# Performance work log

Measured on AMD Instinct MI355X. Metric: run time of the kernel, lower is better.

The kernel has to match this reference:

```python
import jax, jax.numpy as jnp
import numpy as np

GRID = 32
GBOUND = 0.5
GRID_MIN = -GBOUND + GBOUND / GRID  # as in point2voxel


def _voxel_index(points):
    # points: [B,N,3] -> linear voxel indices [B,N]
    vx = (points - GRID_MIN) * GRID / (2.0 * GBOUND)
    vx = jnp.round(jnp.clip(vx, 0.0, GRID - 1))
    lin = vx @ jnp.array([GRID * GRID, GRID, 1], dtype=vx.dtype)
    return lin.astype(jnp.int32)


def _distance_loss(points, cps, v):
    # points [B,N,3], cps [B,G^3,3], v [B,G^3]
    lin = _voxel_index(points)                               # [B,N]
    mask = 1.0 - jnp.take_along_axis(v, lin, axis=1)         # [B,N]
    idx3 = jnp.broadcast_to(lin[:, :, None], lin.shape + (3,))
    gathered = jnp.take_along_axis(cps, idx3, axis=1)        # [B,N,3]
    d = (points - gathered) * mask[:, :, None]
    n2 = jnp.sum(d * d, axis=2)
    norm = jnp.sqrt(jnp.maximum(n2, 1e-30))                  # safe L2 norm
    return jnp.mean(jnp.sum(norm, axis=1))


def _plane_point(p, plane):
    # p [B,N,3], plane [B,1,4] -> reflected points [B,N,3]
    length = 2.0 * (jnp.sum(p * plane[..., :3], axis=2, keepdims=True) + plane[..., 3:4])
    norm2 = jnp.sum(plane[..., :3] ** 2, axis=2, keepdims=True)
    return p - length * plane[..., :3] / (norm2 + 1e-8)


def _quat_mul(q1, q2):
    w1, x1, y1, z1 = q1[..., 0], q1[..., 1], q1[..., 2], q1[..., 3]
    w2, x2, y2, z2 = q2[..., 0], q2[..., 1], q2[..., 2], q2[..., 3]
    w = w1 * w2 - x1 * x2 - y1 * y2 - z1 * z2
    x = w1 * x2 + x1 * w2 + y1 * z2 - z1 * y2
    y = w1 * y2 - x1 * z2 + y1 * w2 + z1 * x2
    z = w1 * z2 + x1 * y2 - y1 * x2 + z1 * w2
    return jnp.stack([w, x, y, z], axis=-1)


def _rotate_point(p, q):
    # p [B,N,3], q [B,1,4]
    B, N, _ = p.shape
    pq = jnp.concatenate([jnp.zeros((B, N, 1), p.dtype), p], axis=-1)
    qc = q * jnp.array([1.0, -1.0, -1.0, -1.0], q.dtype)
    return _quat_mul(_quat_mul(q, pq), qc)[..., 1:]


def setup_inputs() -> dict:
    key = jax.random.key(0)
    k = jax.random.split(key, 5)
    S, B, N, G = 3, 512, 1000, 32
    return {
        "planes": jax.random.normal(k[0], (S, B, 4), dtype=jnp.float32),
        "quats": jax.random.normal(k[1], (S, B, 4), dtype=jnp.float32),
        "closestPoints": jax.random.normal(k[2], (B, G ** 3 * 3), dtype=jnp.float32),
        "surfaceSamples": jax.random.normal(k[3], (B, N, 3), dtype=jnp.float32),
        "volume": jax.random.uniform(k[4], (B, 1, G, G, G), dtype=jnp.float32),
    }


def reference(planes, quats, closestPoints, surfaceSamples, volume):
    B = volume.shape[0]
    v = volume.reshape(B, GRID ** 3)
    cps = closestPoints.reshape(B, -1, 3)

    def per_sym(plane, quat):
        pl = plane[:, None, :]  # [B,1,4]
        lp = _distance_loss(_plane_point(surfaceSamples, pl), cps, v)
        qt = quat[:, None, :]
        lq = _distance_loss(_rotate_point(surfaceSamples, qt), cps, v)
        return lp, lq

    lps, lqs = jax.vmap(per_sym)(planes, quats)  # vectorized over S symmetry elems
    # sum over S then / S == mean, matching the torch loop
    return jnp.mean(lps), jnp.mean(lqs)
```

## Files before the change

### kernel.cpp

```cpp
#include <hip/hip_runtime.h>
#include <math.h>


#define NGRID3     32768
#define GRID_MIN_F (-0.484375f)
#define NTHREADS   256

__device__ __forceinline__ float point_loss(float x, float y, float z,
                                            const float* __restrict__ vol,
                                            const float* __restrict__ cp)
{
    float fx = fminf(fmaxf((x - GRID_MIN_F) * 32.0f, 0.0f), 31.0f);
    float fy = fminf(fmaxf((y - GRID_MIN_F) * 32.0f, 0.0f), 31.0f);
    float fz = fminf(fmaxf((z - GRID_MIN_F) * 32.0f, 0.0f), 31.0f);
    int lin = ((int)rintf(fx)) * 1024 + ((int)rintf(fy)) * 32 + (int)rintf(fz);

    float m  = 1.0f - vol[lin];
    float dx = (x - cp[lin * 3 + 0]) * m;
    float dy = (y - cp[lin * 3 + 1]) * m;
    float dz = (z - cp[lin * 3 + 2]) * m;
    return sqrtf(fmaxf(dx * dx + dy * dy + dz * dz, 1e-30f));
}

template <int S>
__global__ __launch_bounds__(NTHREADS) void symloss_fused(
    const float* __restrict__ planes,
    const float* __restrict__ quats,
    const float* __restrict__ cps,
    const float* __restrict__ samples,
    const float* __restrict__ volume,
    float* __restrict__ out,
    int B, int N, float scale)
{
    const int b = blockIdx.x;
    const float* __restrict__ vol = volume + (size_t)b * NGRID3;
    const float* __restrict__ cp  = cps    + (size_t)b * NGRID3 * 3;

    extern __shared__ float spts[];
    {
        const float* sp = samples + (size_t)b * N * 3;
        const int n4 = (N * 3) / 4;
        const float4* src = (const float4*)sp;
        float4* dst = (float4*)spts;
        for (int i = threadIdx.x; i < n4; i += NTHREADS) dst[i] = src[i];
        for (int i = n4 * 4 + threadIdx.x; i < N * 3; i += NTHREADS) spts[i] = sp[i];
    }

    float plx[S], ply[S], plz[S], plw[S], inv_n2[S];
    float qw[S], qx[S], qy[S], qz[S], w2mu[S];
#pragma unroll
    for (int s = 0; s < S; ++s) {
        float4 pl = ((const float4*)planes)[(size_t)s * B + b];
        float4 q  = ((const float4*)quats )[(size_t)s * B + b];
        plx[s] = pl.x; ply[s] = pl.y; plz[s] = pl.z; plw[s] = pl.w;
        inv_n2[s] = 1.0f / (pl.x * pl.x + pl.y * pl.y + pl.z * pl.z + 1e-8f);
        qw[s] = q.x; qx[s] = q.y; qy[s] = q.z; qz[s] = q.w;
        w2mu[s] = q.x * q.x - (q.y * q.y + q.z * q.z + q.w * q.w);
    }

    __syncthreads();

    float sum_p = 0.0f, sum_q = 0.0f;
    for (int n = threadIdx.x; n < N; n += NTHREADS) {
        const float px = spts[n * 3 + 0];
        const float py = spts[n * 3 + 1];
        const float pz = spts[n * 3 + 2];
#pragma unroll
        for (int s = 0; s < S; ++s) {
            float f = 2.0f * (px * plx[s] + py * ply[s] + pz * plz[s] + plw[s]) * inv_n2[s];
            sum_p += point_loss(px - f * plx[s], py - f * ply[s], pz - f * plz[s], vol, cp);

            float udp = qx[s] * px + qy[s] * py + qz[s] * pz;
            float cx  = qy[s] * pz - qz[s] * py;
            float cy  = qz[s] * px - qx[s] * pz;
            float cz  = qx[s] * py - qy[s] * px;
            sum_q += point_loss(w2mu[s] * px + 2.0f * (udp * qx[s] + qw[s] * cx),
                                w2mu[s] * py + 2.0f * (udp * qy[s] + qw[s] * cy),
                                w2mu[s] * pz + 2.0f * (udp * qz[s] + qw[s] * cz),
                                vol, cp);
        }
    }

    for (int off = 32; off > 0; off >>= 1) {
        sum_p += __shfl_down(sum_p, off);
        sum_q += __shfl_down(sum_q, off);
    }
    __shared__ float red[NTHREADS / 64][2];
    const int lane = threadIdx.x & 63;
    const int wid  = threadIdx.x >> 6;
    if (lane == 0) { red[wid][0] = sum_p; red[wid][1] = sum_q; }
    __syncthreads();

    if (threadIdx.x == 0) {
        float tp = 0.0f, tq = 0.0f;
        for (int w = 0; w < NTHREADS / 64; ++w) { tp += red[w][0]; tq += red[w][1]; }
        atomicAdd(&out[0], tp * scale);
        atomicAdd(&out[1], tq * scale);
    }
}

extern "C" void kernel_launch(void* const* d_in, const int* in_sizes, int n_in,
                              void* d_out, int out_size, void* d_ws, size_t ws_size,
                              hipStream_t stream)
{
    const float* planes  = (const float*)d_in[0];
    const float* quats   = (const float*)d_in[1];
    const float* cps     = (const float*)d_in[2];
    const float* samples = (const float*)d_in[3];
    const float* volume  = (const float*)d_in[4];
    float* out = (float*)d_out;

    const int B = in_sizes[4] / NGRID3;
    const int S = in_sizes[0] / (B * 4);
    const int N = in_sizes[3] / (B * 3);
    const float scale = 1.0f / (float)(S * B);
    const size_t lds = (size_t)N * 3 * sizeof(float);

    hipMemsetAsync(d_out, 0, 2 * sizeof(float), stream);

    switch (S) {
    case 1: symloss_fused<1><<<B, NTHREADS, lds, stream>>>(planes, quats, cps, samples, volume, out, B, N, scale); break;
    case 2: symloss_fused<2><<<B, NTHREADS, lds, stream>>>(planes, quats, cps, samples, volume, out, B, N, scale); break;
    case 3: symloss_fused<3><<<B, NTHREADS, lds, stream>>>(planes, quats, cps, samples, volume, out, B, N, scale); break;
    case 4: symloss_fused<4><<<B, NTHREADS, lds, stream>>>(planes, quats, cps, samples, volume, out, B, N, scale); break;
    default:
        for (int s = 0; s < S; ++s)
            symloss_fused<1><<<B, NTHREADS, lds, stream>>>(planes + (size_t)s * B * 4,
                                                           quats  + (size_t)s * B * 4,
                                                           cps, samples, volume, out, B, N, scale);
        break;
    }
}
```

Baseline: 303.1 us.

## Split each batch over point chunks and reduce partials in a second kernel

Launches C*B blocks, each handling one 256-point chunk of one batch element, instead of one block per batch element. Points are read straight from global memory, so the LDS staging and the barrier go away. Per-block partials go to the workspace and a single-block double-precision reduction kernel replaces the atomics and the memset. The aim is more parallelism to hide the latency of the scattered gathers into the volume and closest-point arrays. The cost is a second launch and less reuse, since blocks working on the same batch element now sit on different CUs.

Measured after the change: 302.0 us. No clear change (-0.3%).

```diff
diff --git a/kernel.cpp b/kernel.cpp
--- a/kernel.cpp
+++ b/kernel.cpp
@@ -16,35 +16,29 @@
     int lin = ((int)rintf(fx)) * 1024 + ((int)rintf(fy)) * 32 + (int)rintf(fz);
 
     float m  = 1.0f - vol[lin];
-    float dx = (x - cp[lin * 3 + 0]) * m;
-    float dy = (y - cp[lin * 3 + 1]) * m;
-    float dz = (z - cp[lin * 3 + 2]) * m;
+    int  c3  = lin * 3;
+    float dx = (x - cp[c3 + 0]) * m;
+    float dy = (y - cp[c3 + 1]) * m;
+    float dz = (z - cp[c3 + 2]) * m;
     return sqrtf(fmaxf(dx * dx + dy * dy + dz * dz, 1e-30f));
 }
 
 template <int S>
-__global__ __launch_bounds__(NTHREADS) void symloss_fused(
+__global__ __launch_bounds__(NTHREADS, 4) void symloss_stage1(
     const float* __restrict__ planes,
     const float* __restrict__ quats,
     const float* __restrict__ cps,
     const float* __restrict__ samples,
     const float* __restrict__ volume,
-    float* __restrict__ out,
-    int B, int N, float scale)
+    float* __restrict__ partials,
+    int B, int N)
 {
-    const int b = blockIdx.x;
+    const int bid = blockIdx.x;
+    const int b   = bid % B;
+    const int c   = bid / B;
+
     const float* __restrict__ vol = volume + (size_t)b * NGRID3;
     const float* __restrict__ cp  = cps    + (size_t)b * NGRID3 * 3;
-
-    extern __shared__ float spts[];
-    {
-        const float* sp = samples + (size_t)b * N * 3;
-        const int n4 = (N * 3) / 4;
-        const float4* src = (const float4*)sp;
-        float4* dst = (float4*)spts;
-        for (int i = threadIdx.x; i < n4; i += NTHREADS) dst[i] = src[i];
-        for (int i = n4 * 4 + threadIdx.x; i < N * 3; i += NTHREADS) spts[i] = sp[i];
-    }
 
     float plx[S], ply[S], plz[S], plw[S], inv_n2[S];
     float qw[S], qx[S], qy[S], qz[S], w2mu[S];
@@ -58,13 +52,13 @@
         w2mu[s] = q.x * q.x - (q.y * q.y + q.z * q.z + q.w * q.w);
     }
 
-    __syncthreads();
-
     float sum_p = 0.0f, sum_q = 0.0f;
-    for (int n = threadIdx.x; n < N; n += NTHREADS) {
-        const float px = spts[n * 3 + 0];
-        const float py = spts[n * 3 + 1];
-        const float pz = spts[n * 3 + 2];
+    const int n = c * NTHREADS + (int)threadIdx.x;
+    if (n < N) {
+        const float* sp = samples + ((size_t)b * N + n) * 3;
+        const float px = sp[0];
+        const float py = sp[1];
+        const float pz = sp[2];
 #pragma unroll
         for (int s = 0; s < S; ++s) {
             float f = 2.0f * (px * plx[s] + py * ply[s] + pz * plz[s] + plw[s]) * inv_n2[s];
@@ -94,8 +88,34 @@
     if (threadIdx.x == 0) {
         float tp = 0.0f, tq = 0.0f;
         for (int w = 0; w < NTHREADS / 64; ++w) { tp += red[w][0]; tq += red[w][1]; }
-        atomicAdd(&out[0], tp * scale);
-        atomicAdd(&out[1], tq * scale);
+        partials[2 * bid + 0] = tp;
+        partials[2 * bid + 1] = tq;
+    }
+}
+
+__global__ __launch_bounds__(NTHREADS) void symloss_reduce(
+    const float* __restrict__ partials, int M, float scale,
+    float* __restrict__ out)
+{
+    double sp = 0.0, sq = 0.0;
+    for (int i = threadIdx.x; i < M; i += NTHREADS) {
+        sp += (double)partials[2 * i + 0];
+        sq += (double)partials[2 * i + 1];
+    }
+    for (int off = 32; off > 0; off >>= 1) {
+        sp += __shfl_down(sp, off);
+        sq += __shfl_down(sq, off);
+    }
+    __shared__ double red[NTHREADS / 64][2];
+    const int lane = threadIdx.x & 63;
+    const int wid  = threadIdx.x >> 6;
+    if (lane == 0) { red[wid][0] = sp; red[wid][1] = sq; }
+    __syncthreads();
+    if (threadIdx.x == 0) {
+        double tp = 0.0, tq = 0.0;
+        for (int w = 0; w < NTHREADS / 64; ++w) { tp += red[w][0]; tq += red[w][1]; }
+        out[0] = (float)(tp * (double)scale);
+        out[1] = (float)(tq * (double)scale);
     }
 }
 
@@ -113,21 +133,25 @@
     const int B = in_sizes[4] / NGRID3;
     const int S = in_sizes[0] / (B * 4);
     const int N = in_sizes[3] / (B * 3);
+    const int C = (N + NTHREADS - 1) / NTHREADS;
     const float scale = 1.0f / (float)(S * B);
-    const size_t lds = (size_t)N * 3 * sizeof(float);
 
-    hipMemsetAsync(d_out, 0, 2 * sizeof(float), stream);
+    float* partials = (float*)d_ws;
+    int M = C * B;
 
     switch (S) {
-    case 1: symloss_fused<1><<<B, NTHREADS, lds, stream>>>(planes, quats, cps, samples, volume, out, B, N, scale); break;
-    case 2: symloss_fused<2><<<B, NTHREADS, lds, stream>>>(planes, quats, cps, samples, volume, out, B, N, scale); break;
-    case 3: symloss_fused<3><<<B, NTHREADS, lds, stream>>>(planes, quats, cps, samples, volume, out, B, N, scale); break;
-    case 4: symloss_fused<4><<<B, NTHREADS, lds, stream>>>(planes, quats, cps, samples, volume, out, B, N, scale); break;
+    case 1: symloss_stage1<1><<<C * B, NTHREADS, 0, stream>>>(planes, quats, cps, samples, volume, partials, B, N); break;
+    case 2: symloss_stage1<2><<<C * B, NTHREADS, 0, stream>>>(planes, quats, cps, samples, volume, partials, B, N); break;
+    case 3: symloss_stage1<3><<<C * B, NTHREADS, 0, stream>>>(planes, quats, cps, samples, volume, partials, B, N); break;
+    case 4: symloss_stage1<4><<<C * B, NTHREADS, 0, stream>>>(planes, quats, cps, samples, volume, partials, B, N); break;
     default:
         for (int s = 0; s < S; ++s)
-            symloss_fused<1><<<B, NTHREADS, lds, stream>>>(planes + (size_t)s * B * 4,
-                                                           quats  + (size_t)s * B * 4,
-                                                           cps, samples, volume, out, B, N, scale);
+            symloss_stage1<1><<<C * B, NTHREADS, 0, stream>>>(
+                planes + (size_t)s * B * 4, quats + (size_t)s * B * 4,
+                cps, samples, volume, partials + (size_t)s * C * B * 2, B, N);
+        M = S * C * B;
         break;
     }
+
+    symloss_reduce<<<1, NTHREADS, 0, stream>>>(partials, M, scale, out);
 }
```
